# Kernel tuning notes

Measured on AMD Instinct MI355X. Metric: run time of the kernel, lower is better.

## Reference

```python
import jax, jax.numpy as jnp
import numpy as np

B, S, H, V_SZ = 256, 49, 2048, 10000

def setup_inputs() -> dict:
    key = jax.random.key(0)
    ks = jax.random.split(key, 24)
    sc = 0.02
    inp = {
        'V': jax.random.normal(ks[0], (B, S, H), jnp.float32),
        'v_g': jax.random.normal(ks[1], (B, H), jnp.float32),
        'state': jax.random.normal(ks[2], (2, 1, B, H), jnp.float32),
        'captions': jax.random.randint(ks[3], (B, 16), 0, V_SZ, jnp.int32),
        'time': 1,
        # params (torch Linear convention: W is (out,in), y = x@W.T+b)
        'fc_W': jax.random.normal(ks[4], (H, H), jnp.float32) * sc,
        'fc_b': jnp.zeros((H,), jnp.float32),
        'att_W': jax.random.normal(ks[5], (H, H), jnp.float32) * sc,
        'att_b': jnp.zeros((H,), jnp.float32),
        'emb': jax.random.normal(ks[6], (V_SZ + 1, H), jnp.float32) * sc,
        'ctx_W': jax.random.normal(ks[7], (H, H), jnp.float32) * sc,
        'ctx_b': jnp.zeros((H,), jnp.float32),
        'a2c_W': jax.random.normal(ks[8], (2 * H, H), jnp.float32) * sc,
        'a2c_b': jnp.zeros((2 * H,), jnp.float32),
        'i2h_W': jax.random.normal(ks[9], (5 * H, H), jnp.float32) * sc,
        'i2h_b': jnp.zeros((5 * H,), jnp.float32),
        'h2h_W': jax.random.normal(ks[10], (5 * H, H), jnp.float32) * sc,
        'h2h_b': jnp.zeros((5 * H,), jnp.float32),
        'h2att_W': jax.random.normal(ks[11], (H, H), jnp.float32) * sc,
        'h2att_b': jnp.zeros((H,), jnp.float32),
        'alpha_W': jax.random.normal(ks[12], (1, H), jnp.float32) * sc,
        'alpha_b': jnp.zeros((1,), jnp.float32),
    }
    return inp


def reference(V, v_g, state, fc_W, fc_b, att_W, att_b, emb, ctx_W, ctx_b,
              a2c_W, a2c_b, i2h_W, i2h_b, h2h_W, h2h_b,
              h2att_W, h2att_b, alpha_W, alpha_b, captions, time):
    # fc_embed(v_g): computed by the original module (unused downstream)
    fc_feats = jax.nn.relu(v_g @ fc_W.T + fc_b)
    # att_embed + ctx2att over the 49 spatial locations
    att_feats = jax.nn.relu(jnp.einsum('bsf,hf->bsh', V, att_W) + att_b)   # (B,49,H)
    p_att = jnp.einsum('bsh,ah->bsa', att_feats, ctx_W) + ctx_b            # (B,49,H)
    # word embedding
    it = captions[:, time]
    xt = jax.nn.relu(emb[it])                                              # (B,H)
    if time == 0:
        state = jnp.zeros_like(state)
    h_prev, c_prev = state[0, -1], state[1, -1]                            # (B,H) each
    # Bahdanau attention
    att_h = h_prev @ h2att_W.T + h2att_b                                   # (B,H)
    dot = jnp.tanh(p_att + att_h[:, None, :])                              # (B,49,H)
    scores = jnp.einsum('bsh,h->bs', dot, alpha_W[0]) + alpha_b[0]         # (B,49)
    weight = jax.nn.softmax(scores, axis=1)
    att_res = jnp.einsum('bs,bsh->bh', weight, att_feats)                  # (B,H)
    # LSTM-with-maxout cell
    sums = xt @ i2h_W.T + i2h_b + h_prev @ h2h_W.T + h2h_b                 # (B,5H)
    Hd = h_prev.shape[-1]
    gates = jax.nn.sigmoid(sums[:, :3 * Hd])
    in_gate, forget_gate, out_gate = gates[:, :Hd], gates[:, Hd:2 * Hd], gates[:, 2 * Hd:]
    in_tr = sums[:, 3 * Hd:] + (att_res @ a2c_W.T + a2c_b)                 # (B,2H)
    in_tr = jnp.maximum(in_tr[:, :Hd], in_tr[:, Hd:])                      # maxout
    next_c = forget_gate * c_prev + in_gate * in_tr
    next_h = out_gate * jnp.tanh(next_c)
    output = next_h[:, None, :]                                            # (B,1,H)
    return output, next_h[None], next_c[None]
```

## Files before the change

### kernel.cpp

```cpp
#include <hip/hip_runtime.h>


typedef __bf16 bf16x8 __attribute__((ext_vector_type(8)));
typedef float  f32x4  __attribute__((ext_vector_type(4)));

static constexpr int Bn = 256;
static constexpr int Sn = 49;
static constexpr int Hn = 2048;
static constexpr int Mrows = Bn * Sn;
static constexpr int LDP = 72;

__device__ __forceinline__ unsigned short f2bf(float f) {
    unsigned u = __builtin_bit_cast(unsigned, f);
    u += 0x7FFFu + ((u >> 16) & 1u);
    return (unsigned short)(u >> 16);
}
__device__ __forceinline__ float bf2f(unsigned short h) {
    return __builtin_bit_cast(float, ((unsigned)h) << 16);
}

__global__ void k_convert(const float* __restrict__ src,
                          unsigned short* __restrict__ dst, int n8) {
    int i = blockIdx.x * blockDim.x + threadIdx.x;
    if (i >= n8) return;
    const float4* p = (const float4*)src + (size_t)i * 2;
    float4 a = p[0], b = p[1];
    union { unsigned short us[8]; int4 v; } o;
    o.us[0] = f2bf(a.x); o.us[1] = f2bf(a.y); o.us[2] = f2bf(a.z); o.us[3] = f2bf(a.w);
    o.us[4] = f2bf(b.x); o.us[5] = f2bf(b.y); o.us[6] = f2bf(b.z); o.us[7] = f2bf(b.w);
    ((int4*)dst)[i] = o.v;
}

__global__ void k_gather(const float* __restrict__ emb,
                         const float* __restrict__ state,
                         const int* __restrict__ captions,
                         const int* __restrict__ timep,
                         unsigned short* __restrict__ xt_b,
                         unsigned short* __restrict__ h_b) {
    int b = blockIdx.x;
    int tm = timep[0];
    int it = captions[b * 16 + tm];
    const float* erow = emb + (size_t)it * Hn;
    for (int h = threadIdx.x; h < Hn; h += blockDim.x) {
        float x = erow[h];
        xt_b[(size_t)b * Hn + h] = f2bf(x > 0.f ? x : 0.f);
        float hv = (tm == 0) ? 0.f : state[(size_t)b * Hn + h];
        h_b[(size_t)b * Hn + h] = f2bf(hv);
    }
}

template<int EPI>
__global__ __launch_bounds__(512, 2)
void k_gemm8(const unsigned short* __restrict__ A,
             const unsigned short* __restrict__ B,
             const float* __restrict__ bias, void* __restrict__ out,
             const float* __restrict__ atth, const float* __restrict__ alphaW,
             int M, int N, int K) {
    __shared__ __align__(16) unsigned short lds[2][2][2][128 * 64];

    const int tid  = threadIdx.x;
    const int lane = tid & 63;
    const int wave = tid >> 6;
    const int wm = wave >> 2;
    const int wn = wave & 3;
    const int wh = wn >> 1;

    const int nm = M >> 8;
    const int wg = (blockIdx.x & 7) * nm + (blockIdx.x >> 3);
    const int m_tile = wg % nm, n_tile = wg / nm;
    const size_t am0 = (size_t)m_tile * 256;
    const size_t bn0 = (size_t)n_tile * 256;

    const int srow = lane >> 3;
    const int scol = (((lane & 7) ^ srow)) * 8;

#define STG(SLOT, G, RBASE, KT)                                              \
    {                                                                        \
        _Pragma("unroll")                                                    \
        for (int j_ = 0; j_ < 2; ++j_) {                                     \
            const int rr_ = (wave * 2 + j_) * 8 + srow;                      \
            const unsigned short* src_ =                                     \
                (G) + ((RBASE) + rr_) * (size_t)K + (KT) * 64 + scol;        \
            __builtin_amdgcn_global_load_lds(                                \
                (const __attribute__((address_space(1))) void*)src_,         \
                (__attribute__((address_space(3))) void*)((SLOT) + (wave * 2 + j_) * 512), \
                16, 0, 0);                                                   \
        }                                                                    \
    }

    unsigned short* SA0_0 = &lds[0][0][0][0];
    unsigned short* SA0_1 = &lds[0][0][1][0];
    unsigned short* SB0_0 = &lds[0][1][0][0];
    unsigned short* SB0_1 = &lds[0][1][1][0];
    unsigned short* SA1_0 = &lds[1][0][0][0];
    unsigned short* SA1_1 = &lds[1][0][1][0];
    unsigned short* SB1_0 = &lds[1][1][0][0];
    unsigned short* SB1_1 = &lds[1][1][1][0];

    const unsigned short* As0r = &lds[0][0][wm][0];
    const unsigned short* As1r = &lds[1][0][wm][0];
    const unsigned short* Bs0r = &lds[0][1][wh][0];
    const unsigned short* Bs1r = &lds[1][1][wh][0];

    const int rfrag = lane & 15;
    const int wnl = (wn & 1) * 64;
    int ck[2];
    ck[0] = (((lane >> 4) * 8)) ^ ((lane & 7) * 8);
    ck[1] = (32 + ((lane >> 4) * 8)) ^ ((lane & 7) * 8);

    f32x4 acc[8][4];
#pragma unroll
    for (int m = 0; m < 8; ++m)
#pragma unroll
        for (int n = 0; n < 4; ++n)
#pragma unroll
            for (int r = 0; r < 4; ++r) acc[m][n][r] = 0.f;

    const int KT_MAX = K / 64 - 1;

    STG(SB0_0, B, bn0 + 0,   0);
    STG(SB0_1, B, bn0 + 128, 0);
    STG(SA0_0, A, am0 + 0,   0);
    STG(SA0_1, A, am0 + 128, 0);
    STG(SB1_0, B, bn0 + 0,   1);
    STG(SB1_1, B, bn0 + 128, 1);
    asm volatile("s_waitcnt vmcnt(4)" ::: "memory");
    __builtin_amdgcn_s_barrier();

    bf16x8 bfr[4][2];

#define PHASE(ASR, BSR, TP, STAGES, TAILWAIT)                                \
    {                                                                        \
        if ((TP) == 0) {                                                     \
            _Pragma("unroll")                                                \
            for (int n = 0; n < 4; ++n) {                                    \
                _Pragma("unroll")                                            \
                for (int s = 0; s < 2; ++s)                                  \
                    bfr[n][s] = *(const bf16x8*)&(BSR)[(wnl + n * 16 + rfrag) * 64 + ck[s]]; \
            }                                                                \
        }                                                                    \
        bf16x8 afr[2][2];                                                    \
        _Pragma("unroll")                                                    \
        for (int mm = 0; mm < 2; ++mm) {                                     \
            _Pragma("unroll")                                                \
            for (int s = 0; s < 2; ++s)                                      \
                afr[mm][s] = *(const bf16x8*)&(ASR)[((2 * (TP) + mm) * 16 + rfrag) * 64 + ck[s]]; \
        }                                                                    \
        STAGES;                                                              \
        __builtin_amdgcn_s_barrier();                                        \
        asm volatile("s_waitcnt lgkmcnt(0)" ::: "memory");                   \
        __builtin_amdgcn_sched_barrier(0);                                   \
        __builtin_amdgcn_s_setprio(1);                                       \
        _Pragma("unroll")                                                    \
        for (int mm = 0; mm < 2; ++mm) {                                     \
            _Pragma("unroll")                                                \
            for (int n = 0; n < 4; ++n) {                                    \
                _Pragma("unroll")                                            \
                for (int s = 0; s < 2; ++s)                                  \
                    acc[2 * (TP) + mm][n] = __builtin_amdgcn_mfma_f32_16x16x32_bf16( \
                        afr[mm][s], bfr[n][s], acc[2 * (TP) + mm][n], 0, 0, 0); \
            }                                                                \
        }                                                                    \
        __builtin_amdgcn_s_setprio(0);                                       \
        TAILWAIT;                                                            \
        __builtin_amdgcn_s_barrier();                                        \
    }

    for (int it = 0; it < K / 128; ++it) {
        const int ktQ  = 2 * it + 1;
        const int ktP2 = (2 * it + 2 < KT_MAX) ? 2 * it + 2 : KT_MAX;
        const int ktQ3 = (2 * it + 3 < KT_MAX) ? 2 * it + 3 : KT_MAX;
        PHASE(As0r, Bs0r, 0, STG(SA1_0, A, am0 + 0, ktQ), );
        PHASE(As0r, Bs0r, 1, { STG(SA1_1, A, am0 + 128, ktQ); STG(SB0_0, B, bn0 + 0, ktP2); }, );
        PHASE(As0r, Bs0r, 2, STG(SB0_1, B, bn0 + 128, ktP2), );
        PHASE(As0r, Bs0r, 3, , asm volatile("s_waitcnt vmcnt(4)" ::: "memory"));
        PHASE(As1r, Bs1r, 0, STG(SA0_0, A, am0 + 0, ktP2), );
        PHASE(As1r, Bs1r, 1, STG(SA0_1, A, am0 + 128, ktP2), );
        PHASE(As1r, Bs1r, 2, STG(SB1_0, B, bn0 + 0, ktQ3), );
        PHASE(As1r, Bs1r, 3, STG(SB1_1, B, bn0 + 128, ktQ3),
              asm volatile("s_waitcnt vmcnt(4)" ::: "memory"));
    }
#undef PHASE
#undef STG

    asm volatile("s_waitcnt vmcnt(0)" ::: "memory");

    const int rq = (lane >> 4) << 2;
#pragma unroll
    for (int m = 0; m < 8; ++m) {
#pragma unroll
        for (int r = 0; r < 4; ++r) {
            const size_t gm = am0 + (size_t)wm * 128 + m * 16 + rq + r;
            if constexpr (EPI == 3) {
                float partial = 0.f;
                const int b = (int)(gm / Sn);
#pragma unroll
                for (int n = 0; n < 4; ++n) {
                    const int gn = (int)bn0 + wn * 64 + n * 16 + rfrag;
                    float v = acc[m][n][r] + bias[gn] + atth[(size_t)b * N + gn];
                    partial += tanhf(v) * alphaW[gn];
                }
#pragma unroll
                for (int off = 1; off < 16; off <<= 1)
                    partial += __shfl_xor(partial, off);
                if (rfrag == 0) atomicAdd(&((float*)out)[gm], partial);
            } else {
#pragma unroll
                for (int n = 0; n < 4; ++n) {
                    const int gn = (int)bn0 + wn * 64 + n * 16 + rfrag;
                    float v = acc[m][n][r] + bias[gn];
                    ((unsigned short*)out)[gm * N + gn] = f2bf(v > 0.f ? v : 0.f);
                }
            }
        }
    }
}

template<bool DUAL>
__global__ __launch_bounds__(256)
void k_gemm_s(const unsigned short* __restrict__ A, const float* __restrict__ B,
              const unsigned short* __restrict__ A2, const float* __restrict__ B2,
              const float* __restrict__ bias, const float* __restrict__ bias2,
              float* __restrict__ out, int M, int N, int K) {
    __shared__ __align__(16) unsigned short As[128 * LDP];
    __shared__ __align__(16) unsigned short Bs[128 * LDP];

    const int tid = threadIdx.x;
    const int m0 = blockIdx.y * 128;
    const int n0 = blockIdx.x * 128;
    const int lane = tid & 63;
    const int wave = tid >> 6;
    const int wm = (wave >> 1) * 64;
    const int wn = (wave & 1) * 64;

    f32x4 acc[4][4];
#pragma unroll
    for (int i = 0; i < 4; ++i)
#pragma unroll
        for (int j = 0; j < 4; ++j)
#pragma unroll
            for (int r = 0; r < 4; ++r) acc[i][j][r] = 0.f;

    const int npass = DUAL ? 2 : 1;
    for (int pass = 0; pass < npass; ++pass) {
        const unsigned short* Ap = pass ? A2 : A;
        const float* Bp = pass ? B2 : B;
        for (int kt = 0; kt < K; kt += 64) {
            __syncthreads();
            {
                const int r = tid >> 3, c = (tid & 7) << 3;
                const unsigned short* src = Ap + (size_t)(m0 + r) * K + kt + c;
#pragma unroll
                for (int i = 0; i < 4; ++i) {
                    int4 v = *(const int4*)(src + (size_t)i * 32 * K);
                    *(int4*)&As[(r + i * 32) * LDP + c] = v;
                }
            }
            {
                const int r = tid >> 4, c = (tid & 15) << 2;
                const float* src = Bp + (size_t)(n0 + r) * K + kt + c;
#pragma unroll
                for (int i = 0; i < 8; ++i) {
                    float4 v = *(const float4*)(src + (size_t)i * 16 * K);
                    union { unsigned short us[4]; uint2 u2; } t;
                    t.us[0] = f2bf(v.x); t.us[1] = f2bf(v.y);
                    t.us[2] = f2bf(v.z); t.us[3] = f2bf(v.w);
                    *(uint2*)&Bs[(r + i * 16) * LDP + c] = t.u2;
                }
            }
            __syncthreads();
#pragma unroll
            for (int ks = 0; ks < 64; ks += 32) {
                const int col = ks + ((lane >> 4) << 3);
                const int ra = wm + (lane & 15);
                const int rb = wn + (lane & 15);
                bf16x8 af[4], bfr[4];
#pragma unroll
                for (int i = 0; i < 4; ++i)
                    af[i] = *(const bf16x8*)&As[(ra + i * 16) * LDP + col];
#pragma unroll
                for (int j = 0; j < 4; ++j)
                    bfr[j] = *(const bf16x8*)&Bs[(rb + j * 16) * LDP + col];
#pragma unroll
                for (int i = 0; i < 4; ++i)
#pragma unroll
                    for (int j = 0; j < 4; ++j)
                        acc[i][j] = __builtin_amdgcn_mfma_f32_16x16x32_bf16(
                            af[i], bfr[j], acc[i][j], 0, 0, 0);
            }
        }
    }

#pragma unroll
    for (int i = 0; i < 4; ++i) {
#pragma unroll
        for (int r = 0; r < 4; ++r) {
            const int gm = m0 + wm + i * 16 + ((lane >> 4) << 2) + r;
#pragma unroll
            for (int j = 0; j < 4; ++j) {
                const int gn = n0 + wn + j * 16 + (lane & 15);
                float v = acc[i][j][r] + bias[gn];
                if (DUAL) v += bias2[gn];
                out[(size_t)gm * N + gn] = v;
            }
        }
    }
}

__global__ void k_softmax(const float* __restrict__ scores, float* __restrict__ weight) {
    int b = blockIdx.x;
    int s = threadIdx.x;
    float v = (s < Sn) ? scores[b * Sn + s] : -1e30f;
    float m = v;
#pragma unroll
    for (int off = 1; off < 64; off <<= 1) m = fmaxf(m, __shfl_xor(m, off));
    float e = (s < Sn) ? __expf(v - m) : 0.f;
    float sum = e;
#pragma unroll
    for (int off = 1; off < 64; off <<= 1) sum += __shfl_xor(sum, off);
    if (s < Sn) weight[b * Sn + s] = e / sum;
}

__global__ void k_attres(const float* __restrict__ weight,
                         const unsigned short* __restrict__ attf,
                         unsigned short* __restrict__ attres) {
    int b = blockIdx.y;
    int h = blockIdx.x * blockDim.x + threadIdx.x;
    const unsigned short* p = attf + (size_t)b * Sn * Hn + h;
    float acc = 0.f;
#pragma unroll 7
    for (int s = 0; s < Sn; ++s)
        acc += weight[b * Sn + s] * bf2f(p[(size_t)s * Hn]);
    attres[(size_t)b * Hn + h] = f2bf(acc);
}

__global__ void k_final(const float* __restrict__ sums, const float* __restrict__ a2c,
                        const float* __restrict__ state, const int* __restrict__ timep,
                        float* __restrict__ out) {
    int idx = blockIdx.x * blockDim.x + threadIdx.x;
    int b = idx >> 11, h = idx & (Hn - 1);
    const float* srow = sums + (size_t)b * 5 * Hn;
    float ig = 1.f / (1.f + __expf(-srow[h]));
    float fg = 1.f / (1.f + __expf(-srow[Hn + h]));
    float og = 1.f / (1.f + __expf(-srow[2 * Hn + h]));
    float t1 = srow[3 * Hn + h] + a2c[(size_t)b * 2 * Hn + h];
    float t2 = srow[4 * Hn + h] + a2c[(size_t)b * 2 * Hn + Hn + h];
    float intr = fmaxf(t1, t2);
    float cprev = (timep[0] == 0) ? 0.f : state[(size_t)Bn * Hn + idx];
    float c = fg * cprev + ig * intr;
    float hh = og * tanhf(c);
    const int BH = Bn * Hn;
    out[idx] = hh;
    out[BH + idx] = hh;
    out[2 * BH + idx] = c;
}

extern "C" void kernel_launch(void* const* d_in, const int* in_sizes, int n_in,
                              void* d_out, int out_size, void* d_ws, size_t ws_size,
                              hipStream_t stream) {
    const float* V        = (const float*)d_in[0];
    const float* state    = (const float*)d_in[2];
    const int*   captions = (const int*)d_in[3];
    const int*   timep    = (const int*)d_in[4];
    const float* att_W    = (const float*)d_in[7];
    const float* att_b    = (const float*)d_in[8];
    const float* emb      = (const float*)d_in[9];
    const float* ctx_W    = (const float*)d_in[10];
    const float* ctx_b    = (const float*)d_in[11];
    const float* a2c_W    = (const float*)d_in[12];
    const float* a2c_b    = (const float*)d_in[13];
    const float* i2h_W    = (const float*)d_in[14];
    const float* i2h_b    = (const float*)d_in[15];
    const float* h2h_W    = (const float*)d_in[16];
    const float* h2h_b    = (const float*)d_in[17];
    const float* h2att_W  = (const float*)d_in[18];
    const float* h2att_b  = (const float*)d_in[19];
    const float* alpha_W  = (const float*)d_in[20];

    unsigned short* Vb      = (unsigned short*)d_ws;
    unsigned short* attWb   = Vb + (size_t)Mrows * Hn;
    unsigned short* ctxWb   = attWb + (size_t)Hn * Hn;
    unsigned short* attfb   = ctxWb + (size_t)Hn * Hn;
    unsigned short* xtb     = attfb + (size_t)Mrows * Hn;
    unsigned short* hb      = xtb + Bn * Hn;
    unsigned short* attresb = hb + Bn * Hn;
    float* atth    = (float*)(attresb + Bn * Hn);
    float* scores  = atth + Bn * Hn;
    float* weight  = scores + Mrows;
    float* sums    = weight + Mrows;
    float* a2c_out = sums + (size_t)Bn * 5 * Hn;

    hipMemsetAsync(scores, 0, Mrows * sizeof(float), stream);

    k_convert<<<(Mrows * Hn / 8) / 256, 256, 0, stream>>>(V, Vb, Mrows * Hn / 8);
    k_convert<<<(Hn * Hn / 8) / 256, 256, 0, stream>>>(att_W, attWb, Hn * Hn / 8);
    k_convert<<<(Hn * Hn / 8) / 256, 256, 0, stream>>>(ctx_W, ctxWb, Hn * Hn / 8);
    k_gather<<<Bn, 256, 0, stream>>>(emb, state, captions, timep, xtb, hb);

    const int nwg = (Mrows / 256) * (Hn / 256);

    k_gemm8<0><<<nwg, 512, 0, stream>>>(
        Vb, attWb, att_b, attfb, nullptr, nullptr, Mrows, Hn, Hn);
    k_gemm_s<false><<<dim3(Hn / 128, Bn / 128), 256, 0, stream>>>(
        hb, h2att_W, nullptr, nullptr, h2att_b, nullptr, atth, Bn, Hn, Hn);
    k_gemm8<3><<<nwg, 512, 0, stream>>>(
        attfb, ctxWb, ctx_b, scores, atth, alpha_W, Mrows, Hn, Hn);
    k_softmax<<<Bn, 64, 0, stream>>>(scores, weight);
    k_attres<<<dim3(Hn / 256, Bn), 256, 0, stream>>>(weight, attfb, attresb);
    k_gemm_s<true><<<dim3(5 * Hn / 128, Bn / 128), 256, 0, stream>>>(
        xtb, i2h_W, hb, h2h_W, i2h_b, h2h_b, sums, Bn, 5 * Hn, Hn);
    k_gemm_s<false><<<dim3(2 * Hn / 128, Bn / 128), 256, 0, stream>>>(
        attresb, a2c_W, nullptr, nullptr, a2c_b, nullptr, a2c_out, Bn, 2 * Hn, Hn);

    k_final<<<Bn * Hn / 256, 256, 0, stream>>>(sums, a2c_out, state, timep, (float*)d_out);
}
```

Before: 571.9 us.

## Software-pipeline LDS fragment reads one phase ahead of MFMA in GEMM loop

Restructures the GEMM main loop so the A fragments for the next phase, and the B fragments for the next half-tile, are read from LDS while the current phase's MFMAs run. Two sets of fragment registers are used in ping-pong fashion. This hides LDS read latency and drops one barrier per phase. The global-to-LDS stage schedule is also reordered to fit the new scheme. The cost is more live VGPRs, which may lower occupancy or cause spills, and the new ordering carries hazard risk on the LDS buffers.

```diff
diff --git a/kernel.cpp b/kernel.cpp
--- a/kernel.cpp
+++ b/kernel.cpp
@@ -104,9 +104,8 @@
 
     const int rfrag = lane & 15;
     const int wnl = (wn & 1) * 64;
-    int ck[2];
-    ck[0] = (((lane >> 4) * 8)) ^ ((lane & 7) * 8);
-    ck[1] = (32 + ((lane >> 4) * 8)) ^ ((lane & 7) * 8);
+    const int ck0 = (((lane >> 4) * 8)) ^ ((lane & 7) * 8);
+    const int ck1 = (32 + ((lane >> 4) * 8)) ^ ((lane & 7) * 8);
 
     f32x4 acc[8][4];
 #pragma unroll
@@ -116,72 +115,105 @@
 #pragma unroll
             for (int r = 0; r < 4; ++r) acc[m][n][r] = 0.f;
 
-    const int KT_MAX = K / 64 - 1;
+    bf16x8 bfrP[4][2], bfrQ[4][2], pf0[2][2], pf1[2][2];
+
+#define RDA(ASR, TP, PF)                                                     \
+    _Pragma("unroll")                                                        \
+    for (int mm = 0; mm < 2; ++mm) {                                         \
+        PF[mm][0] = *(const bf16x8*)&(ASR)[((2 * (TP) + mm) * 16 + rfrag) * 64 + ck0]; \
+        PF[mm][1] = *(const bf16x8*)&(ASR)[((2 * (TP) + mm) * 16 + rfrag) * 64 + ck1]; \
+    }
+#define RDB(BSR, BF)                                                         \
+    _Pragma("unroll")                                                        \
+    for (int n = 0; n < 4; ++n) {                                            \
+        BF[n][0] = *(const bf16x8*)&(BSR)[(wnl + n * 16 + rfrag) * 64 + ck0]; \
+        BF[n][1] = *(const bf16x8*)&(BSR)[(wnl + n * 16 + rfrag) * 64 + ck1]; \
+    }
+#define MM(PF, BF, TP)                                                       \
+    __builtin_amdgcn_s_setprio(1);                                           \
+    _Pragma("unroll")                                                        \
+    for (int mm = 0; mm < 2; ++mm)                                           \
+        _Pragma("unroll")                                                    \
+        for (int n = 0; n < 4; ++n)                                          \
+            _Pragma("unroll")                                                \
+            for (int s = 0; s < 2; ++s)                                      \
+                acc[2 * (TP) + mm][n] = __builtin_amdgcn_mfma_f32_16x16x32_bf16( \
+                    PF[mm][s], BF[n][s], acc[2 * (TP) + mm][n], 0, 0, 0);    \
+    __builtin_amdgcn_s_setprio(0);
+
+#define FENCE  __builtin_amdgcn_sched_barrier(0)
+#define LGKM0  asm volatile("s_waitcnt lgkmcnt(0)" ::: "memory")
+#define VM4    asm volatile("s_waitcnt vmcnt(4)" ::: "memory")
+#define BAR    __builtin_amdgcn_s_barrier()
 
     STG(SB0_0, B, bn0 + 0,   0);
     STG(SB0_1, B, bn0 + 128, 0);
     STG(SA0_0, A, am0 + 0,   0);
     STG(SA0_1, A, am0 + 128, 0);
+    asm volatile("s_waitcnt vmcnt(0)" ::: "memory");
+    BAR;
+    RDB(Bs0r, bfrP);
+    RDA(As0r, 0, pf0);
     STG(SB1_0, B, bn0 + 0,   1);
     STG(SB1_1, B, bn0 + 128, 1);
-    asm volatile("s_waitcnt vmcnt(4)" ::: "memory");
-    __builtin_amdgcn_s_barrier();
-
-    bf16x8 bfr[4][2];
-
-#define PHASE(ASR, BSR, TP, STAGES, TAILWAIT)                                \
-    {                                                                        \
-        if ((TP) == 0) {                                                     \
-            _Pragma("unroll")                                                \
-            for (int n = 0; n < 4; ++n) {                                    \
-                _Pragma("unroll")                                            \
-                for (int s = 0; s < 2; ++s)                                  \
-                    bfr[n][s] = *(const bf16x8*)&(BSR)[(wnl + n * 16 + rfrag) * 64 + ck[s]]; \
-            }                                                                \
-        }                                                                    \
-        bf16x8 afr[2][2];                                                    \
-        _Pragma("unroll")                                                    \
-        for (int mm = 0; mm < 2; ++mm) {                                     \
-            _Pragma("unroll")                                                \
-            for (int s = 0; s < 2; ++s)                                      \
-                afr[mm][s] = *(const bf16x8*)&(ASR)[((2 * (TP) + mm) * 16 + rfrag) * 64 + ck[s]]; \
-        }                                                                    \
-        STAGES;                                                              \
-        __builtin_amdgcn_s_barrier();                                        \
-        asm volatile("s_waitcnt lgkmcnt(0)" ::: "memory");                   \
-        __builtin_amdgcn_sched_barrier(0);                                   \
-        __builtin_amdgcn_s_setprio(1);                                       \
-        _Pragma("unroll")                                                    \
-        for (int mm = 0; mm < 2; ++mm) {                                     \
-            _Pragma("unroll")                                                \
-            for (int n = 0; n < 4; ++n) {                                    \
-                _Pragma("unroll")                                            \
-                for (int s = 0; s < 2; ++s)                                  \
-                    acc[2 * (TP) + mm][n] = __builtin_amdgcn_mfma_f32_16x16x32_bf16( \
-                        afr[mm][s], bfr[n][s], acc[2 * (TP) + mm][n], 0, 0, 0); \
-            }                                                                \
-        }                                                                    \
-        __builtin_amdgcn_s_setprio(0);                                       \
-        TAILWAIT;                                                            \
-        __builtin_amdgcn_s_barrier();                                        \
-    }
-
+    STG(SA1_0, A, am0 + 0,   1);
+    STG(SA1_1, A, am0 + 128, 1);
+    LGKM0;
+    BAR;
+
+    const int KT_MAX = K / 64 - 1;
     for (int it = 0; it < K / 128; ++it) {
-        const int ktQ  = 2 * it + 1;
         const int ktP2 = (2 * it + 2 < KT_MAX) ? 2 * it + 2 : KT_MAX;
         const int ktQ3 = (2 * it + 3 < KT_MAX) ? 2 * it + 3 : KT_MAX;
-        PHASE(As0r, Bs0r, 0, STG(SA1_0, A, am0 + 0, ktQ), );
-        PHASE(As0r, Bs0r, 1, { STG(SA1_1, A, am0 + 128, ktQ); STG(SB0_0, B, bn0 + 0, ktP2); }, );
-        PHASE(As0r, Bs0r, 2, STG(SB0_1, B, bn0 + 128, ktP2), );
-        PHASE(As0r, Bs0r, 3, , asm volatile("s_waitcnt vmcnt(4)" ::: "memory"));
-        PHASE(As1r, Bs1r, 0, STG(SA0_0, A, am0 + 0, ktP2), );
-        PHASE(As1r, Bs1r, 1, STG(SA0_1, A, am0 + 128, ktP2), );
-        PHASE(As1r, Bs1r, 2, STG(SB1_0, B, bn0 + 0, ktQ3), );
-        PHASE(As1r, Bs1r, 3, STG(SB1_1, B, bn0 + 128, ktQ3),
-              asm volatile("s_waitcnt vmcnt(4)" ::: "memory"));
-    }
-#undef PHASE
+        RDA(As0r, 1, pf1); FENCE;
+        MM(pf0, bfrP, 0);
+        LGKM0; FENCE;
+        STG(SB0_0, B, bn0 + 0, ktP2);
+        BAR;
+        RDA(As0r, 2, pf0); FENCE;
+        MM(pf1, bfrP, 1);
+        LGKM0; FENCE;
+        STG(SB0_1, B, bn0 + 128, ktP2);
+        BAR;
+        RDA(As0r, 3, pf1); FENCE;
+        MM(pf0, bfrP, 2);
+        LGKM0; FENCE;
+        VM4;
+        BAR;
+        RDB(Bs1r, bfrQ);
+        RDA(As1r, 0, pf0); FENCE;
+        MM(pf1, bfrP, 3);
+        LGKM0; FENCE;
+        STG(SA0_0, A, am0 + 0, ktP2);
+        BAR;
+        RDA(As1r, 1, pf1); FENCE;
+        MM(pf0, bfrQ, 0);
+        LGKM0; FENCE;
+        STG(SA0_1, A, am0 + 128, ktP2);
+        STG(SB1_0, B, bn0 + 0, ktQ3);
+        BAR;
+        RDA(As1r, 2, pf0); FENCE;
+        MM(pf1, bfrQ, 1);
+        LGKM0; FENCE;
+        STG(SB1_1, B, bn0 + 128, ktQ3);
+        BAR;
+        RDA(As1r, 3, pf1); FENCE;
+        MM(pf0, bfrQ, 2);
+        LGKM0; FENCE;
+        VM4;
+        BAR;
+        RDB(Bs0r, bfrP);
+        RDA(As0r, 0, pf0); FENCE;
+        MM(pf1, bfrQ, 3);
+        LGKM0; FENCE;
+        STG(SA1_0, A, am0 + 0, ktQ3);
+        STG(SA1_1, A, am0 + 128, ktQ3);
+        BAR;
+    }
 #undef STG
+#undef RDA
+#undef RDB
+#undef MM
 
     asm volatile("s_waitcnt vmcnt(0)" ::: "memory");
 
```

After: 719.4 us. 1.26x slower.
